# Performance work log

Measured on AMD Instinct MI355X. Metric: run time of the kernel, lower is better.

The kernel has to match this reference:

```python
import jax, jax.numpy as jnp
import numpy as np

EPS = 0.07      # sinkhorn temperature
ITERS = 7       # sinkhorn iterations
TINY = 1e-8
NORM_EPS = 1e-12  # F.normalize default clamp


def setup_inputs() -> dict:
    key = jax.random.key(0)
    k1, k2 = jax.random.split(key)
    x = jax.random.normal(k1, (64, 2048, 24, 12), dtype=jnp.float32)
    anchors = jax.random.normal(k2, (2, 2048), dtype=jnp.float32) * 0.02
    return {"x": x, "anchors": anchors}


def reference(x, anchors):
    B, C, H, W = x.shape
    HW = H * W
    # tokens: (B, HW, C)
    X = x.reshape(B, C, HW).transpose(0, 2, 1)
    Xn = X / jnp.maximum(jnp.linalg.norm(X, axis=-1, keepdims=True), NORM_EPS)
    An = anchors / jnp.maximum(jnp.linalg.norm(anchors, axis=-1, keepdims=True), NORM_EPS)
    # cosine cost (B, HW, 2)
    Cmat = 1.0 - jnp.einsum('bhc,kc->bhk', Xn, An)
    Kmat = jnp.exp(-Cmat / max(EPS, TINY)) + TINY
    a = jnp.full((B, HW), 1.0 / HW, dtype=Kmat.dtype)
    b = jnp.full((B, 2), 0.5, dtype=Kmat.dtype)

    def step(carry, _):
        u, v = carry
        Kv = jnp.einsum('bhk,bk->bh', Kmat, v) + TINY
        u = a / Kv
        KTu = jnp.einsum('bhk,bh->bk', Kmat, u) + TINY
        v = b / KTu
        return (u, v), None

    u0 = jnp.ones((B, HW), dtype=Kmat.dtype)
    v0 = jnp.ones((B, 2), dtype=Kmat.dtype)
    (u, v), _ = jax.lax.scan(step, (u0, v0), None, length=ITERS)
    # transport plan and soft masks
    P = Kmat * u[:, :, None] * v[:, None, :]          # (B, HW, 2)
    m = (P * HW).transpose(0, 2, 1).reshape(B, 2, H, W)
    # masked pooling for both prototypes at once
    num = jnp.einsum('bchw,bkhw->bkc', x, m)           # (B, 2, C)
    den = m.sum(axis=(2, 3)) + 1e-6                    # (B, 2)
    c = num / den[:, :, None]
    c0_vec = c[:, 0][:, :, None, None]                 # (B, C, 1, 1)
    c1_vec = c[:, 1][:, :, None, None]
    return (c0_vec, c1_vec, m)
```

## Files before the change

### kernel.cpp

```cpp
#include <hip/hip_runtime.h>

#define B_    64
#define C_    2048
#define HW_   288
#define EPS_  0.07f
#define TINY_ 1e-8f
#define NCH_  64
#define CPC_  (C_ / NCH_)

__device__ __forceinline__ float comp(const float4 v, int i) {
  return i == 0 ? v.x : i == 1 ? v.y : i == 2 ? v.z : v.w;
}

__device__ __forceinline__ void acc3(const float4 v, float a0, float a1,
                                     float* ssq, float* sd0, float* sd1) {
  ssq[0] += v.x * v.x; ssq[1] += v.y * v.y; ssq[2] += v.z * v.z; ssq[3] += v.w * v.w;
  sd0[0] += v.x * a0;  sd0[1] += v.y * a0;  sd0[2] += v.z * a0;  sd0[3] += v.w * a0;
  sd1[0] += v.x * a1;  sd1[1] += v.y * a1;  sd1[2] += v.z * a1;  sd1[3] += v.w * a1;
}

__global__ __launch_bounds__(256) void k1_partials(
    const float* __restrict__ x, const float* __restrict__ anchors,
    float* __restrict__ part) {
  int bi = blockIdx.x;
  int b  = bi >> 4;
  int cg = bi & 15;
  int t = threadIdx.x, lane = t & 63, wid = t >> 6;
  int ch = cg * 4 + wid;
  int c0 = ch * CPC_;
  const float* xb = x + ((size_t)b * C_ + c0) * HW_;
  const float4* a0v = (const float4*)(anchors + c0);
  const float4* a1v = (const float4*)(anchors + C_ + c0);

  float ssq[4] = {0,0,0,0}, sd0[4] = {0,0,0,0}, sd1[4] = {0,0,0,0};

  float4 xbuf[4], abuf0, abuf1;
#pragma unroll
  for (int j = 0; j < 4; ++j)
    xbuf[j] = ((const float4*)(xb + (size_t)j * HW_))[lane];
  abuf0 = a0v[0];
  abuf1 = a1v[0];

#pragma unroll 1
  for (int r = 0; r < CPC_; r += 4) {
    float4 xcur[4], ac0 = abuf0, ac1 = abuf1;
#pragma unroll
    for (int j = 0; j < 4; ++j) xcur[j] = xbuf[j];
    if (r + 4 < CPC_) {
#pragma unroll
      for (int j = 0; j < 4; ++j)
        xbuf[j] = ((const float4*)(xb + (size_t)(r + 4 + j) * HW_))[lane];
      abuf0 = a0v[(r >> 2) + 1];
      abuf1 = a1v[(r >> 2) + 1];
    }
#pragma unroll
    for (int j = 0; j < 4; ++j)
      acc3(xcur[j], comp(ac0, j), comp(ac1, j), ssq, sd0, sd1);
  }

  int rg = lane >> 3, q = lane & 7;
  float4 tv[4];
  float ta0[4], ta1[4];
#pragma unroll
  for (int k = 0; k < CPC_ / 8; ++k) {
    int r = k * 8 + rg;
    tv[k]  = ((const float4*)(xb + (size_t)r * HW_))[64 + q];
    ta0[k] = anchors[c0 + r];
    ta1[k] = anchors[C_ + c0 + r];
  }
  float tsq[4] = {0,0,0,0}, td0[4] = {0,0,0,0}, td1[4] = {0,0,0,0};
#pragma unroll
  for (int k = 0; k < CPC_ / 8; ++k)
    acc3(tv[k], ta0[k], ta1[k], tsq, td0, td1);
#pragma unroll
  for (int off = 8; off < 64; off <<= 1) {
#pragma unroll
    for (int j = 0; j < 4; ++j) {
      tsq[j] += __shfl_xor(tsq[j], off);
      td0[j] += __shfl_xor(td0[j], off);
      td1[j] += __shfl_xor(td1[j], off);
    }
  }

  size_t PS = (size_t)B_ * NCH_ * HW_;
  float* base = part + (size_t)(b * NCH_ + ch) * HW_;
  ((float4*)base)[lane]          = make_float4(ssq[0], ssq[1], ssq[2], ssq[3]);
  ((float4*)(base + PS))[lane]   = make_float4(sd0[0], sd0[1], sd0[2], sd0[3]);
  ((float4*)(base + 2*PS))[lane] = make_float4(sd1[0], sd1[1], sd1[2], sd1[3]);
  if (lane < 8) {
    ((float4*)base)[64 + lane]          = make_float4(tsq[0], tsq[1], tsq[2], tsq[3]);
    ((float4*)(base + PS))[64 + lane]   = make_float4(td0[0], td0[1], td0[2], td0[3]);
    ((float4*)(base + 2*PS))[64 + lane] = make_float4(td1[0], td1[1], td1[2], td1[3]);
  }
}

__device__ __forceinline__ void block_reduce2(
    float& p0, float& p1, volatile float* red0, volatile float* red1,
    int t, int nw) {
  int lane = t & 63, wid = t >> 6;
#pragma unroll
  for (int off = 32; off >= 1; off >>= 1) {
    p0 += __shfl_down(p0, off);
    p1 += __shfl_down(p1, off);
  }
  __syncthreads();
  if (lane == 0) { red0[wid] = p0; red1[wid] = p1; }
  __syncthreads();
  float s0 = 0.f, s1 = 0.f;
  for (int w = 0; w < nw; ++w) { s0 += red0[w]; s1 += red1[w]; }
  p0 = s0; p1 = s1;
}

__global__ __launch_bounds__(320) void k2_sinkhorn(
    const float* __restrict__ part, const float* __restrict__ anchors,
    float* __restrict__ out_m, float* __restrict__ invden) {
  int b = blockIdx.x, t = threadIdx.x;
  __shared__ float red0[8], red1[8];
  const int nw = 5;

  float a0 = 0.f, a1 = 0.f;
  for (int c = t; c < C_; c += 320) {
    float q0 = anchors[c], q1 = anchors[C_ + c];
    a0 += q0 * q0; a1 += q1 * q1;
  }
  block_reduce2(a0, a1, red0, red1, t, nw);
  float ian0 = 1.0f / fmaxf(sqrtf(a0), 1e-12f);
  float ian1 = 1.0f / fmaxf(sqrtf(a1), 1e-12f);

  float K0 = 0.f, K1 = 0.f;
  if (t < HW_) {
    size_t PS = (size_t)B_ * NCH_ * HW_;
    const float* p = part + (size_t)b * NCH_ * HW_ + t;
    float ssq = 0.f, d0 = 0.f, d1 = 0.f;
#pragma unroll 8
    for (int ch = 0; ch < NCH_; ++ch) {
      size_t o = (size_t)ch * HW_;
      ssq += p[o];
      d0  += p[PS + o];
      d1  += p[2 * PS + o];
    }
    float ixn = 1.0f / fmaxf(sqrtf(ssq), 1e-12f);
    K0 = expf((d0 * ixn * ian0 - 1.0f) / EPS_) + TINY_;
    K1 = expf((d1 * ixn * ian1 - 1.0f) / EPS_) + TINY_;
  }

  float v0 = 1.f, v1 = 1.f, u = 0.f;
  for (int it = 0; it < 7; ++it) {
    if (t < HW_) u = (1.0f / (float)HW_) / (K0 * v0 + K1 * v1 + TINY_);
    float p0 = K0 * u, p1 = K1 * u;
    block_reduce2(p0, p1, red0, red1, t, nw);
    v0 = 0.5f / (p0 + TINY_);
    v1 = 0.5f / (p1 + TINY_);
  }

  float m0 = 0.f, m1 = 0.f;
  if (t < HW_) {
    m0 = K0 * u * v0 * (float)HW_;
    m1 = K1 * u * v1 * (float)HW_;
  }
  float q0 = m0, q1 = m1;
  block_reduce2(q0, q1, red0, red1, t, nw);
  if (t < HW_) {
    out_m[(b * 2 + 0) * HW_ + t] = m0;
    out_m[(b * 2 + 1) * HW_ + t] = m1;
  }
  if (t == 0) {
    invden[b * 2 + 0] = 1.0f / (q0 + 1e-6f);
    invden[b * 2 + 1] = 1.0f / (q1 + 1e-6f);
  }
}

__global__ __launch_bounds__(256) void k3_pool(
    const float* __restrict__ x, const float* __restrict__ m,
    const float* __restrict__ invden, float* __restrict__ out) {
  int bi = blockIdx.x;
  int b = bi >> 4, seg = bi & 15;
  int t = threadIdx.x, oct = t & 7, rl = t >> 3;

  const float4* m0 = (const float4*)(m + (b * 2 + 0) * HW_);
  const float4* m1 = (const float4*)(m + (b * 2 + 1) * HW_);
  float4 w0[9], w1[9];
#pragma unroll
  for (int j = 0; j < 9; ++j) {
    w0[j] = m0[oct + 8 * j];
    w1[j] = m1[oct + 8 * j];
  }
  float inv0 = invden[2 * b], inv1 = invden[2 * b + 1];

  int cbase = seg * 128;
#pragma unroll 1
  for (int g = 0; g < 4; ++g) {
    int c = cbase + g * 32 + rl;
    const float4* xr = (const float4*)(x + ((size_t)b * C_ + c) * HW_);
    float4 xa[9];
#pragma unroll
    for (int j = 0; j < 9; ++j) xa[j] = xr[oct + 8 * j];
    float a0 = 0.f, a1 = 0.f;
#pragma unroll
    for (int j = 0; j < 9; ++j) {
      a0 += xa[j].x * w0[j].x + xa[j].y * w0[j].y + xa[j].z * w0[j].z + xa[j].w * w0[j].w;
      a1 += xa[j].x * w1[j].x + xa[j].y * w1[j].y + xa[j].z * w1[j].z + xa[j].w * w1[j].w;
    }
#pragma unroll
    for (int off = 4; off >= 1; off >>= 1) {
      a0 += __shfl_xor(a0, off);
      a1 += __shfl_xor(a1, off);
    }
    if (oct == 0) {
      out[(size_t)b * C_ + c] = a0 * inv0;
      out[(size_t)B_ * C_ + (size_t)b * C_ + c] = a1 * inv1;
    }
  }
}

extern "C" void kernel_launch(void* const* d_in, const int* in_sizes, int n_in,
                              void* d_out, int out_size, void* d_ws, size_t ws_size,
                              hipStream_t stream) {
  const float* x       = (const float*)d_in[0];
  const float* anchors = (const float*)d_in[1];
  float* out = (float*)d_out;

  float* invden = (float*)d_ws;
  float* part = invden + 128;

  float* out_m = out + 2 * B_ * C_;

  k1_partials<<<B_ * (NCH_ / 4), 256, 0, stream>>>(x, anchors, part);
  k2_sinkhorn<<<B_, 320, 0, stream>>>(part, anchors, out_m, invden);
  k3_pool<<<B_ * 16, 256, 0, stream>>>(x, out_m, invden, out);
}
```

Measured before the change: 249.7 us.

## Fuse three kernels into one cooperative persistent kernel with grid syncs

Replaces the three launches with a single cooperative kernel that runs the partial-sum pass, a grid-wide reduction of partials, the per-batch Sinkhorn solve and the pooling pass, separated by grid.sync. The reduction over channel partials is now spread across the whole grid instead of done by only 64 blocks, and the partial-sum loop is reworked into a fully unrolled double-buffered prefetch of 8 rows. This aims to remove launch gaps and the serial partial reduction in the Sinkhorn kernel. In exchange it pays for grid-wide barriers, the Sinkhorn phase runs on only 64 blocks while the rest of the grid idles, and the grid is capped by occupancy, which limits parallelism in the streaming phases.

```diff
diff --git a/kernel.cpp b/kernel.cpp
--- a/kernel.cpp
+++ b/kernel.cpp
@@ -1,4 +1,7 @@
 #include <hip/hip_runtime.h>
+#include <hip/hip_cooperative_groups.h>
+
+namespace cg = cooperative_groups;
 
 #define B_    64
 #define C_    2048
@@ -7,6 +10,7 @@
 #define TINY_ 1e-8f
 #define NCH_  64
 #define CPC_  (C_ / NCH_)
+#define NJOB_ (B_ * 16)
 
 __device__ __forceinline__ float comp(const float4 v, int i) {
   return i == 0 ? v.x : i == 1 ? v.y : i == 2 ? v.z : v.w;
@@ -19,14 +23,13 @@
   sd1[0] += v.x * a1;  sd1[1] += v.y * a1;  sd1[2] += v.z * a1;  sd1[3] += v.w * a1;
 }
 
-__global__ __launch_bounds__(256) void k1_partials(
+__device__ __forceinline__ void p1_body(
     const float* __restrict__ x, const float* __restrict__ anchors,
-    float* __restrict__ part) {
-  int bi = blockIdx.x;
+    float* __restrict__ part, int bi, int t) {
   int b  = bi >> 4;
-  int cg = bi & 15;
-  int t = threadIdx.x, lane = t & 63, wid = t >> 6;
-  int ch = cg * 4 + wid;
+  int cg_ = bi & 15;
+  int lane = t & 63, wid = t >> 6;
+  int ch = cg_ * 4 + wid;
   int c0 = ch * CPC_;
   const float* xb = x + ((size_t)b * C_ + c0) * HW_;
   const float4* a0v = (const float4*)(anchors + c0);
@@ -34,28 +37,27 @@
 
   float ssq[4] = {0,0,0,0}, sd0[4] = {0,0,0,0}, sd1[4] = {0,0,0,0};
 
-  float4 xbuf[4], abuf0, abuf1;
-#pragma unroll
-  for (int j = 0; j < 4; ++j)
-    xbuf[j] = ((const float4*)(xb + (size_t)j * HW_))[lane];
-  abuf0 = a0v[0];
-  abuf1 = a1v[0];
-
-#pragma unroll 1
-  for (int r = 0; r < CPC_; r += 4) {
-    float4 xcur[4], ac0 = abuf0, ac1 = abuf1;
-#pragma unroll
-    for (int j = 0; j < 4; ++j) xcur[j] = xbuf[j];
-    if (r + 4 < CPC_) {
-#pragma unroll
-      for (int j = 0; j < 4; ++j)
-        xbuf[j] = ((const float4*)(xb + (size_t)(r + 4 + j) * HW_))[lane];
-      abuf0 = a0v[(r >> 2) + 1];
-      abuf1 = a1v[(r >> 2) + 1];
-    }
-#pragma unroll
-    for (int j = 0; j < 4; ++j)
-      acc3(xcur[j], comp(ac0, j), comp(ac1, j), ssq, sd0, sd1);
+  float4 bufX[2][8], bufA[2][4];
+#pragma unroll
+  for (int j = 0; j < 8; ++j)
+    bufX[0][j] = ((const float4*)(xb + (size_t)j * HW_))[lane];
+  bufA[0][0] = a0v[0]; bufA[0][1] = a0v[1];
+  bufA[0][2] = a1v[0]; bufA[0][3] = a1v[1];
+
+#pragma unroll
+  for (int g = 0; g < CPC_ / 8; ++g) {
+    const int cur = g & 1, nxt = cur ^ 1;
+    if (g + 1 < CPC_ / 8) {
+#pragma unroll
+      for (int j = 0; j < 8; ++j)
+        bufX[nxt][j] = ((const float4*)(xb + (size_t)((g + 1) * 8 + j) * HW_))[lane];
+      bufA[nxt][0] = a0v[2 * (g + 1)];     bufA[nxt][1] = a0v[2 * (g + 1) + 1];
+      bufA[nxt][2] = a1v[2 * (g + 1)];     bufA[nxt][3] = a1v[2 * (g + 1) + 1];
+    }
+#pragma unroll
+    for (int j = 0; j < 8; ++j)
+      acc3(bufX[cur][j], comp(bufA[cur][j >> 2], j & 3),
+           comp(bufA[cur][2 + (j >> 2)], j & 3), ssq, sd0, sd1);
   }
 
   int rg = lane >> 3, q = lane & 7;
@@ -94,9 +96,51 @@
   }
 }
 
+__device__ __forceinline__ void p3_body(
+    const float* __restrict__ x, const float* __restrict__ m,
+    const float* __restrict__ invden, float* __restrict__ out, int bi, int t) {
+  int b = bi >> 4, seg = bi & 15;
+  int oct = t & 7, rl = t >> 3;
+
+  const float4* m0 = (const float4*)(m + (b * 2 + 0) * HW_);
+  const float4* m1 = (const float4*)(m + (b * 2 + 1) * HW_);
+  float4 w0[9], w1[9];
+#pragma unroll
+  for (int j = 0; j < 9; ++j) {
+    w0[j] = m0[oct + 8 * j];
+    w1[j] = m1[oct + 8 * j];
+  }
+  float inv0 = invden[2 * b], inv1 = invden[2 * b + 1];
+
+  int cbase = seg * 128;
+#pragma unroll 1
+  for (int g = 0; g < 4; ++g) {
+    int c = cbase + g * 32 + rl;
+    const float4* xr = (const float4*)(x + ((size_t)b * C_ + c) * HW_);
+    float4 xa[9];
+#pragma unroll
+    for (int j = 0; j < 9; ++j) xa[j] = xr[oct + 8 * j];
+    float a0 = 0.f, a1 = 0.f;
+#pragma unroll
+    for (int j = 0; j < 9; ++j) {
+      a0 += xa[j].x * w0[j].x + xa[j].y * w0[j].y + xa[j].z * w0[j].z + xa[j].w * w0[j].w;
+      a1 += xa[j].x * w1[j].x + xa[j].y * w1[j].y + xa[j].z * w1[j].z + xa[j].w * w1[j].w;
+    }
+#pragma unroll
+    for (int off = 4; off >= 1; off >>= 1) {
+      a0 += __shfl_xor(a0, off);
+      a1 += __shfl_xor(a1, off);
+    }
+    if (oct == 0) {
+      out[(size_t)b * C_ + c] = a0 * inv0;
+      out[(size_t)B_ * C_ + (size_t)b * C_ + c] = a1 * inv1;
+    }
+  }
+}
+
+template <int NW>
 __device__ __forceinline__ void block_reduce2(
-    float& p0, float& p1, volatile float* red0, volatile float* red1,
-    int t, int nw) {
+    float& p0, float& p1, volatile float* r0, volatile float* r1, int t) {
   int lane = t & 63, wid = t >> 6;
 #pragma unroll
   for (int off = 32; off >= 1; off >>= 1) {
@@ -104,11 +148,119 @@
     p1 += __shfl_down(p1, off);
   }
   __syncthreads();
-  if (lane == 0) { red0[wid] = p0; red1[wid] = p1; }
+  if (lane == 0) { r0[wid] = p0; r1[wid] = p1; }
   __syncthreads();
   float s0 = 0.f, s1 = 0.f;
-  for (int w = 0; w < nw; ++w) { s0 += red0[w]; s1 += red1[w]; }
+#pragma unroll
+  for (int w = 0; w < NW; ++w) { s0 += r0[w]; s1 += r1[w]; }
   p0 = s0; p1 = s1;
+}
+
+__global__ __launch_bounds__(256, 4) void mega(
+    const float* __restrict__ x, const float* __restrict__ anchors,
+    float* __restrict__ part, float* __restrict__ invden,
+    float* __restrict__ out) {
+  cg::grid_group grid = cg::this_grid();
+  __shared__ float s_r0[4], s_r1[4];
+  int t = threadIdx.x;
+  float* out_m = out + 2 * B_ * C_;
+
+  for (int bi = blockIdx.x; bi < NJOB_; bi += gridDim.x)
+    p1_body(x, anchors, part, bi, t);
+
+  grid.sync();
+
+  {
+    float* red = invden + 128 + 0;
+    for (int idx = blockIdx.x * 256 + t; idx < 3 * B_ * HW_;
+         idx += gridDim.x * 256) {
+      int plane = idx / (B_ * HW_);
+      int rem = idx - plane * (B_ * HW_);
+      int b = rem / HW_;
+      int h = rem - b * HW_;
+      const float* p = part + (size_t)plane * B_ * NCH_ * HW_
+                            + (size_t)b * NCH_ * HW_ + h;
+      float s = 0.f;
+#pragma unroll 8
+      for (int ch = 0; ch < NCH_; ++ch) s += p[(size_t)ch * HW_];
+      red[idx] = s;
+    }
+  }
+
+  grid.sync();
+
+  for (int b = blockIdx.x; b < B_; b += gridDim.x) {
+    const float* red = invden + 128;
+    float a0 = 0.f, a1 = 0.f;
+    for (int c = t; c < C_; c += 256) {
+      float q0 = anchors[c], q1 = anchors[C_ + c];
+      a0 += q0 * q0; a1 += q1 * q1;
+    }
+    block_reduce2<4>(a0, a1, s_r0, s_r1, t);
+    float ian0 = 1.0f / fmaxf(sqrtf(a0), 1e-12f);
+    float ian1 = 1.0f / fmaxf(sqrtf(a1), 1e-12f);
+
+    bool hb = t < (HW_ - 256);
+    float Ka0, Ka1, Kb0 = 0.f, Kb1 = 0.f;
+    {
+      float ssq = red[b * HW_ + t];
+      float d0  = red[B_ * HW_ + b * HW_ + t];
+      float d1  = red[2 * B_ * HW_ + b * HW_ + t];
+      float ixn = 1.0f / fmaxf(sqrtf(ssq), 1e-12f);
+      Ka0 = expf((d0 * ixn * ian0 - 1.0f) / EPS_) + TINY_;
+      Ka1 = expf((d1 * ixn * ian1 - 1.0f) / EPS_) + TINY_;
+    }
+    if (hb) {
+      int h = 256 + t;
+      float ssq = red[b * HW_ + h];
+      float d0  = red[B_ * HW_ + b * HW_ + h];
+      float d1  = red[2 * B_ * HW_ + b * HW_ + h];
+      float ixn = 1.0f / fmaxf(sqrtf(ssq), 1e-12f);
+      Kb0 = expf((d0 * ixn * ian0 - 1.0f) / EPS_) + TINY_;
+      Kb1 = expf((d1 * ixn * ian1 - 1.0f) / EPS_) + TINY_;
+    }
+
+    float v0 = 1.f, v1 = 1.f, ua = 0.f, ub = 0.f;
+    const float ia = 1.0f / (float)HW_;
+    for (int it = 0; it < 7; ++it) {
+      ua = ia / (Ka0 * v0 + Ka1 * v1 + TINY_);
+      ub = ia / (Kb0 * v0 + Kb1 * v1 + TINY_);
+      float p0 = Ka0 * ua + (hb ? Kb0 * ub : 0.f);
+      float p1 = Ka1 * ua + (hb ? Kb1 * ub : 0.f);
+      block_reduce2<4>(p0, p1, s_r0, s_r1, t);
+      v0 = 0.5f / (p0 + TINY_);
+      v1 = 0.5f / (p1 + TINY_);
+    }
+
+    float ma0 = Ka0 * ua * v0 * (float)HW_;
+    float ma1 = Ka1 * ua * v1 * (float)HW_;
+    float mb0 = hb ? Kb0 * ub * v0 * (float)HW_ : 0.f;
+    float mb1 = hb ? Kb1 * ub * v1 * (float)HW_ : 0.f;
+    float q0 = ma0 + mb0, q1 = ma1 + mb1;
+    block_reduce2<4>(q0, q1, s_r0, s_r1, t);
+
+    out_m[(b * 2 + 0) * HW_ + t] = ma0;
+    out_m[(b * 2 + 1) * HW_ + t] = ma1;
+    if (hb) {
+      out_m[(b * 2 + 0) * HW_ + 256 + t] = mb0;
+      out_m[(b * 2 + 1) * HW_ + 256 + t] = mb1;
+    }
+    if (t == 0) {
+      invden[b * 2 + 0] = 1.0f / (q0 + 1e-6f);
+      invden[b * 2 + 1] = 1.0f / (q1 + 1e-6f);
+    }
+  }
+
+  grid.sync();
+
+  for (int bi = blockIdx.x; bi < NJOB_; bi += gridDim.x)
+    p3_body(x, out_m, invden, out, bi, t);
+}
+
+__global__ __launch_bounds__(256) void k1_partials(
+    const float* __restrict__ x, const float* __restrict__ anchors,
+    float* __restrict__ part) {
+  p1_body(x, anchors, part, blockIdx.x, threadIdx.x);
 }
 
 __global__ __launch_bounds__(320) void k2_sinkhorn(
@@ -116,14 +268,13 @@
     float* __restrict__ out_m, float* __restrict__ invden) {
   int b = blockIdx.x, t = threadIdx.x;
   __shared__ float red0[8], red1[8];
-  const int nw = 5;
 
   float a0 = 0.f, a1 = 0.f;
   for (int c = t; c < C_; c += 320) {
     float q0 = anchors[c], q1 = anchors[C_ + c];
     a0 += q0 * q0; a1 += q1 * q1;
   }
-  block_reduce2(a0, a1, red0, red1, t, nw);
+  block_reduce2<5>(a0, a1, red0, red1, t);
   float ian0 = 1.0f / fmaxf(sqrtf(a0), 1e-12f);
   float ian1 = 1.0f / fmaxf(sqrtf(a1), 1e-12f);
 
@@ -148,7 +299,7 @@
   for (int it = 0; it < 7; ++it) {
     if (t < HW_) u = (1.0f / (float)HW_) / (K0 * v0 + K1 * v1 + TINY_);
     float p0 = K0 * u, p1 = K1 * u;
-    block_reduce2(p0, p1, red0, red1, t, nw);
+    block_reduce2<5>(p0, p1, red0, red1, t);
     v0 = 0.5f / (p0 + TINY_);
     v1 = 0.5f / (p1 + TINY_);
   }
@@ -159,7 +310,7 @@
     m1 = K1 * u * v1 * (float)HW_;
   }
   float q0 = m0, q1 = m1;
-  block_reduce2(q0, q1, red0, red1, t, nw);
+  block_reduce2<5>(q0, q1, red0, red1, t);
   if (t < HW_) {
     out_m[(b * 2 + 0) * HW_ + t] = m0;
     out_m[(b * 2 + 1) * HW_ + t] = m1;
@@ -173,44 +324,7 @@
 __global__ __launch_bounds__(256) void k3_pool(
     const float* __restrict__ x, const float* __restrict__ m,
     const float* __restrict__ invden, float* __restrict__ out) {
-  int bi = blockIdx.x;
-  int b = bi >> 4, seg = bi & 15;
-  int t = threadIdx.x, oct = t & 7, rl = t >> 3;
-
-  const float4* m0 = (const float4*)(m + (b * 2 + 0) * HW_);
-  const float4* m1 = (const float4*)(m + (b * 2 + 1) * HW_);
-  float4 w0[9], w1[9];
-#pragma unroll
-  for (int j = 0; j < 9; ++j) {
-    w0[j] = m0[oct + 8 * j];
-    w1[j] = m1[oct + 8 * j];
-  }
-  float inv0 = invden[2 * b], inv1 = invden[2 * b + 1];
-
-  int cbase = seg * 128;
-#pragma unroll 1
-  for (int g = 0; g < 4; ++g) {
-    int c = cbase + g * 32 + rl;
-    const float4* xr = (const float4*)(x + ((size_t)b * C_ + c) * HW_);
-    float4 xa[9];
-#pragma unroll
-    for (int j = 0; j < 9; ++j) xa[j] = xr[oct + 8 * j];
-    float a0 = 0.f, a1 = 0.f;
-#pragma unroll
-    for (int j = 0; j < 9; ++j) {
-      a0 += xa[j].x * w0[j].x + xa[j].y * w0[j].y + xa[j].z * w0[j].z + xa[j].w * w0[j].w;
-      a1 += xa[j].x * w1[j].x + xa[j].y * w1[j].y + xa[j].z * w1[j].z + xa[j].w * w1[j].w;
-    }
-#pragma unroll
-    for (int off = 4; off >= 1; off >>= 1) {
-      a0 += __shfl_xor(a0, off);
-      a1 += __shfl_xor(a1, off);
-    }
-    if (oct == 0) {
-      out[(size_t)b * C_ + c] = a0 * inv0;
-      out[(size_t)B_ * C_ + (size_t)b * C_ + c] = a1 * inv1;
-    }
-  }
+  p3_body(x, m, invden, out, blockIdx.x, threadIdx.x);
 }
 
 extern "C" void kernel_launch(void* const* d_in, const int* in_sizes, int n_in,
@@ -221,11 +335,25 @@
   float* out = (float*)d_out;
 
   float* invden = (float*)d_ws;
-  float* part = invden + 128;
-
+  float* part = invden + 128 + 3 * B_ * HW_;
   float* out_m = out + 2 * B_ * C_;
 
-  k1_partials<<<B_ * (NCH_ / 4), 256, 0, stream>>>(x, anchors, part);
-  k2_sinkhorn<<<B_, 320, 0, stream>>>(part, anchors, out_m, invden);
-  k3_pool<<<B_ * 16, 256, 0, stream>>>(x, out_m, invden, out);
-}
+  int blocksPerCU = 0;
+  hipError_t e = hipOccupancyMaxActiveBlocksPerMultiprocessor(
+      &blocksPerCU, (const void*)mega, 256, 0);
+  bool coop_ok = (e == hipSuccess && blocksPerCU > 0);
+  if (coop_ok) {
+    int maxBlocks = blocksPerCU * 256;
+    int gridSize = maxBlocks < NJOB_ ? maxBlocks : NJOB_;
+    void* args[] = {(void*)&x, (void*)&anchors, (void*)&part,
+                    (void*)&invden, (void*)&out};
+    e = hipLaunchCooperativeKernel((const void*)mega, dim3(gridSize), dim3(256),
+                                   args, 0, stream);
+    coop_ok = (e == hipSuccess);
+  }
+  if (!coop_ok) {
+    k1_partials<<<NJOB_, 256, 0, stream>>>(x, anchors, part);
+    k2_sinkhorn<<<B_, 320, 0, stream>>>(part, anchors, out_m, invden);
+    k3_pool<<<NJOB_, 256, 0, stream>>>(x, out_m, invden, out);
+  }
+}
```

Result: slower. 423.2 us (+69.5%).
